# Kernel tuning notes

Measured on AMD Instinct MI355X. Metric: run time of the kernel, lower is better.

The kernel has to match this reference:

```python
import jax, jax.numpy as jnp
import numpy as np

T, B, I, H = 512, 32, 512, 512

def setup_inputs() -> dict:
    key = jax.random.key(0)
    k1, k2, k3 = jax.random.split(key, 3)
    x = jax.random.normal(k1, (T, B, I), dtype=jnp.float32)
    h0 = jnp.zeros((B, H), dtype=jnp.float32)
    W_ih = jax.random.normal(k2, (3 * H, I), dtype=jnp.float32) * (1.0 / np.sqrt(H))
    # diagonal recurrent weights, one vector per gate (r, z, n), uniform(-1, 1)
    w_hh = jax.random.uniform(k3, (3, H), dtype=jnp.float32, minval=-1.0, maxval=1.0)
    return {"x": x, "h0": h0, "W_ih": W_ih, "w_hh": w_hh}

def reference(x, h0, W_ih, w_hh):
    # Precompute input-side gate pre-activations for all timesteps: (T, B, 3H)
    gx = jnp.einsum('tbi,gi->tbg', x, W_ih)
    xr, xz, xn = jnp.split(gx, 3, axis=-1)  # each (T, B, H)
    w_r, w_z, w_n = w_hh[0], w_hh[1], w_hh[2]  # each (H,)

    def step(h, g):
        gr, gz, gn = g
        r = jax.nn.sigmoid(gr + w_r * h)
        z = jax.nn.sigmoid(gz + w_z * h)
        n = jnp.tanh(gn + r * (w_n * h))
        h_new = (1.0 - z) * n + z * h
        return h_new, h_new

    h_last, out = jax.lax.scan(step, h0, (xr, xz, xn))
    # out: (T, B, H) all hidden states; h_last: (1, B, H) final state (GRU convention)
    return out, h_last[None, :, :]
```

## Files before the change

### kernel.cpp

```cpp
#include <hip/hip_runtime.h>
#include <hip/hip_bf16.h>
#include <stdint.h>

#define T_DIM 512
#define B_DIM 32
#define K_DIM 512
#define H_DIM 512
#define N_DIM 1536
#define M_DIM 16384

typedef __bf16 bf16_t;
typedef bf16_t bf16x8 __attribute__((ext_vector_type(8)));
typedef float floatx4 __attribute__((ext_vector_type(4)));

#define LOG2E 1.442695041f
#define TWO_LOG2E 2.885390082f

__device__ __forceinline__ unsigned int f2bf_bits(float f) {
  uint32_t u = __builtin_bit_cast(uint32_t, f);
  u += 0x7FFFu + ((u >> 16) & 1u);
  return u >> 16;
}

__global__ void convert_both_kernel(const float* __restrict__ x,
                                    unsigned short* __restrict__ xb,
                                    const float* __restrict__ W,
                                    unsigned short* __restrict__ Wb) {
  int bid = blockIdx.x;
  const float* src;
  unsigned short* dst;
  int i;
  if (bid < 4096) {
    i = (bid * 256 + threadIdx.x) * 8;
    src = x + i;
    dst = xb + i;
  } else {
    i = ((bid - 4096) * 256 + threadIdx.x) * 8;
    int n = i >> 9;
    int k = i & 511;
    int p6 = n / 6;
    int sub = n - p6 * 6;
    int hodd = (sub >= 3) ? 1 : 0;
    int g = sub - hodd * 3;
    int h = p6 * 2 + hodd;
    src = W + ((g << 9) + h) * 512 + k;
    dst = Wb + i;
  }
  const float4* p = (const float4*)src;
  float4 f0 = p[0];
  float4 f1 = p[1];
  uint4 v;
  v.x = f2bf_bits(f0.x) | (f2bf_bits(f0.y) << 16);
  v.y = f2bf_bits(f0.z) | (f2bf_bits(f0.w) << 16);
  v.z = f2bf_bits(f1.x) | (f2bf_bits(f1.y) << 16);
  v.w = f2bf_bits(f1.z) | (f2bf_bits(f1.w) << 16);
  *(uint4*)dst = v;
}

__global__ __launch_bounds__(512, 4) void gemm_bf16_kernel(
    const unsigned short* __restrict__ A, const unsigned short* __restrict__ Bm,
    _Float16* __restrict__ C) {
  __shared__ bf16_t smem[24576];
  const int tid = threadIdx.x;
  const int lane = tid & 63;
  const int w = tid >> 6;
  const int id = blockIdx.x;
  const int swz = (id & 7) * 96 + (id >> 3);
  const int mIdx = swz / 12;
  const int nIdx = swz - mIdx * 12;
  const int tileM = mIdx * 256;
  const int tileN = nIdx * 128;
  const int waveM = w & 3;
  const int waveN = w >> 2;
  const int lm = lane & 15;
  const int lg = lane >> 4;

  floatx4 acc[4][4] = {};

  for (int k0 = 0; k0 < K_DIM; k0 += 64) {
#pragma unroll
    for (int g = 0; g < 4; ++g) {
      int s = g * 512 + tid;
      int row = s >> 3;
      int kc = (s & 7) ^ (row & 7);
      bf16_t* la = smem + (g * 512 + w * 64) * 8;
      const unsigned short* ga = A + (size_t)(tileM + row) * K_DIM + k0 + kc * 8;
      __builtin_amdgcn_global_load_lds(
          (const __attribute__((address_space(1))) unsigned int*)ga,
          (__attribute__((address_space(3))) unsigned int*)la, 16, 0, 0);
    }
#pragma unroll
    for (int g = 0; g < 2; ++g) {
      int s = g * 512 + tid;
      int row = s >> 3;
      int kc = (s & 7) ^ (row & 7);
      bf16_t* lb = smem + 16384 + (g * 512 + w * 64) * 8;
      const unsigned short* gb = Bm + (size_t)(tileN + row) * K_DIM + k0 + kc * 8;
      __builtin_amdgcn_global_load_lds(
          (const __attribute__((address_space(1))) unsigned int*)gb,
          (__attribute__((address_space(3))) unsigned int*)lb, 16, 0, 0);
    }
    __syncthreads();

#pragma unroll
    for (int ks = 0; ks < 2; ++ks) {
      bf16x8 af[4], bfg[4];
#pragma unroll
      for (int i = 0; i < 4; ++i) {
        int row = waveM * 64 + i * 16 + lm;
        int c = ks * 4 + lg;
        af[i] = *(const bf16x8*)(smem + row * 64 + (c ^ (row & 7)) * 8);
      }
#pragma unroll
      for (int j = 0; j < 4; ++j) {
        int row = waveN * 64 + j * 16 + lm;
        int c = ks * 4 + lg;
        bfg[j] = *(const bf16x8*)(smem + 16384 + row * 64 + (c ^ (row & 7)) * 8);
      }
#pragma unroll
      for (int i = 0; i < 4; ++i)
#pragma unroll
        for (int j = 0; j < 4; ++j)
          acc[i][j] = __builtin_amdgcn_mfma_f32_16x16x32_bf16(af[i], bfg[j],
                                                              acc[i][j], 0, 0, 0);
    }
    __syncthreads();
  }

  _Float16* ep = (_Float16*)smem + w * 2048;
  const int q = lm;
  const int rgrp = lane >> 4;
  const size_t crow0 = (size_t)(tileM + waveM * 64);
  const int ccol = tileN + waveN * 64 + q * 4;
#pragma unroll
  for (int p = 0; p < 2; ++p) {
#pragma unroll
    for (int il = 0; il < 2; ++il) {
      const int i = 2 * p + il;
#pragma unroll
      for (int j = 0; j < 4; ++j) {
        const int cl = lm + j * 16;
        const int sub = (tileN + waveN * 64 + cl) % 6;
        const float scl = (sub == 2 || sub == 5) ? TWO_LOG2E : -LOG2E;
#pragma unroll
        for (int r = 0; r < 4; ++r) {
          int rl = (lane >> 4) * 4 + r + 16 * il;
          ep[rl * 64 + cl] = (_Float16)(scl * acc[i][j][r]);
        }
      }
    }
#pragma unroll
    for (int k = 0; k < 8; ++k) {
      int rl = rgrp + 4 * k;
      uint2 v = *(const uint2*)(ep + rl * 64 + q * 4);
      *(uint2*)(C + (crow0 + p * 32 + rl) * N_DIM + ccol) = v;
    }
  }
}

__global__ __launch_bounds__(64) void indgru_scan_kernel(
    const _Float16* __restrict__ gx, const float* __restrict__ h0,
    const float* __restrict__ w_hh, float* __restrict__ out,
    float* __restrict__ hlast) {
  const int idx = blockIdx.x * 64 + threadIdx.x;
  const int b = idx >> 9;
  const int h = idx & (H_DIM - 1);
  const float wr = -LOG2E * w_hh[h];
  const float wz = -LOG2E * w_hh[H_DIM + h];
  const float wn = TWO_LOG2E * w_hh[2 * H_DIM + h];
  const int sh = (h & 1) << 4;
  float hv = h0[idx];

  const char* base = (const char*)(gx + (size_t)b * N_DIM + (h >> 1) * 6) + ((h & 1) << 2);
  float* outp = out + (size_t)b * H_DIM + h;

  constexpr int D = 32;
  constexpr size_t TSTRIDE = (size_t)B_DIM * N_DIM * sizeof(_Float16);
  uint2 pq[D];
#pragma unroll
  for (int t = 0; t < D; ++t)
    pq[t] = *(const uint2*)(base + (size_t)t * TSTRIDE);

  auto cvt16 = [](uint32_t bits) {
    return (float)__builtin_bit_cast(_Float16, (unsigned short)bits);
  };

  for (int t0 = 0; t0 < T_DIM - D; t0 += D) {
#pragma unroll
    for (int s = 0; s < D; ++s) {
      const int t = t0 + s;
      uint2 qv = pq[s];
      pq[s] = *(const uint2*)(base + (size_t)(t + D) * TSTRIDE);
      asm volatile("" ::: "memory");
      uint64_t v = (((uint64_t)qv.y << 32) | qv.x) >> sh;
      float gr = cvt16((uint32_t)v);
      float gz = cvt16((uint32_t)(v >> 16));
      float gn = cvt16((uint32_t)(v >> 32));
      float ar = fmaf(wr, hv, gr);
      float az = fmaf(wz, hv, gz);
      float t1 = wn * hv;
      float er = __builtin_amdgcn_exp2f(ar);
      float ez = __builtin_amdgcn_exp2f(az);
      float r = __builtin_amdgcn_rcpf(1.0f + er);
      float z = __builtin_amdgcn_rcpf(1.0f + ez);
      float en = __builtin_amdgcn_exp2f(fmaf(r, t1, gn));
      float u = __builtin_amdgcn_rcpf(1.0f + en);
      float n = fmaf(-2.0f, u, 1.0f);
      float zh = z * hv;
      float omz = 1.0f - z;
      hv = fmaf(n, omz, zh);
      outp[(size_t)t * (B_DIM * H_DIM)] = hv;
    }
  }
#pragma unroll
  for (int s = 0; s < D; ++s) {
    const int t = T_DIM - D + s;
    uint2 qv = pq[s];
    uint64_t v = (((uint64_t)qv.y << 32) | qv.x) >> sh;
    float gr = cvt16((uint32_t)v);
    float gz = cvt16((uint32_t)(v >> 16));
    float gn = cvt16((uint32_t)(v >> 32));
    float ar = fmaf(wr, hv, gr);
    float az = fmaf(wz, hv, gz);
    float t1 = wn * hv;
    float er = __builtin_amdgcn_exp2f(ar);
    float ez = __builtin_amdgcn_exp2f(az);
    float r = __builtin_amdgcn_rcpf(1.0f + er);
    float z = __builtin_amdgcn_rcpf(1.0f + ez);
    float en = __builtin_amdgcn_exp2f(fmaf(r, t1, gn));
    float u = __builtin_amdgcn_rcpf(1.0f + en);
    float n = fmaf(-2.0f, u, 1.0f);
    float zh = z * hv;
    float omz = 1.0f - z;
    hv = fmaf(n, omz, zh);
    outp[(size_t)t * (B_DIM * H_DIM)] = hv;
  }
  hlast[idx] = hv;
}

extern "C" void kernel_launch(void* const* d_in, const int* in_sizes, int n_in,
                              void* d_out, int out_size, void* d_ws, size_t ws_size,
                              hipStream_t stream) {
  const float* x    = (const float*)d_in[0];
  const float* h0   = (const float*)d_in[1];
  const float* W_ih = (const float*)d_in[2];
  const float* w_hh = (const float*)d_in[3];

  float* out = (float*)d_out;
  float* hlast = out + (size_t)T_DIM * B_DIM * H_DIM;

  char* ws = (char*)d_ws;
  unsigned short* xb = (unsigned short*)ws;
  unsigned short* Wb = (unsigned short*)(ws + 16777216);
  _Float16* gx = (_Float16*)(ws + 16777216 + 1572864);

  convert_both_kernel<<<4480, 256, 0, stream>>>(x, xb, W_ih, Wb);

  gemm_bf16_kernel<<<768, 512, 0, stream>>>(xb, Wb, gx);

  indgru_scan_kernel<<<256, 64, 0, stream>>>(gx, h0, w_hh, out, hlast);
}
```

Before: 149.9 us.

## Enlarge GEMM tile to 256x384 with 2x4 wave layout and 256 blocks

The GEMM block tile grows from 256x128 to 256x384. Each wave now computes a 128x96 sub-tile, 8x6 MFMA accumulators, with the A fragment loaded inside the row loop. The grid shrinks to 256 blocks, about one per CU, so A is reloaded fewer times across N tiles and MFMA work per LDS load rises. In exchange, register pressure is much higher, LDS per block grows, occupancy drops to 2 blocks, and the epilogue is restructured with padded staging rows.

```diff
diff --git a/kernel.cpp b/kernel.cpp
--- a/kernel.cpp
+++ b/kernel.cpp
@@ -57,25 +57,25 @@
   *(uint4*)dst = v;
 }
 
-__global__ __launch_bounds__(512, 4) void gemm_bf16_kernel(
+__global__ __launch_bounds__(512, 2) void gemm_bf16_kernel(
     const unsigned short* __restrict__ A, const unsigned short* __restrict__ Bm,
     _Float16* __restrict__ C) {
-  __shared__ bf16_t smem[24576];
+  __shared__ bf16_t smem[40960];
   const int tid = threadIdx.x;
   const int lane = tid & 63;
   const int w = tid >> 6;
   const int id = blockIdx.x;
-  const int swz = (id & 7) * 96 + (id >> 3);
-  const int mIdx = swz / 12;
-  const int nIdx = swz - mIdx * 12;
+  const int swz = (id & 7) * 32 + (id >> 3);
+  const int mIdx = swz >> 2;
+  const int nIdx = swz & 3;
   const int tileM = mIdx * 256;
-  const int tileN = nIdx * 128;
-  const int waveM = w & 3;
-  const int waveN = w >> 2;
+  const int tileN = nIdx * 384;
+  const int waveM = w >> 2;
+  const int waveN = w & 3;
   const int lm = lane & 15;
   const int lg = lane >> 4;
 
-  floatx4 acc[4][4] = {};
+  floatx4 acc[8][6] = {};
 
   for (int k0 = 0; k0 < K_DIM; k0 += 64) {
 #pragma unroll
@@ -90,7 +90,7 @@
           (__attribute__((address_space(3))) unsigned int*)la, 16, 0, 0);
     }
 #pragma unroll
-    for (int g = 0; g < 2; ++g) {
+    for (int g = 0; g < 6; ++g) {
       int s = g * 512 + tid;
       int row = s >> 3;
       int kc = (s & 7) ^ (row & 7);
@@ -104,56 +104,53 @@
 
 #pragma unroll
     for (int ks = 0; ks < 2; ++ks) {
-      bf16x8 af[4], bfg[4];
-#pragma unroll
-      for (int i = 0; i < 4; ++i) {
-        int row = waveM * 64 + i * 16 + lm;
-        int c = ks * 4 + lg;
-        af[i] = *(const bf16x8*)(smem + row * 64 + (c ^ (row & 7)) * 8);
+      bf16x8 bfg[6];
+      const int c = ks * 4 + lg;
+#pragma unroll
+      for (int j = 0; j < 6; ++j) {
+        int row = waveN * 96 + j * 16 + lm;
+        bfg[j] = *(const bf16x8*)(smem + 16384 + row * 64 + ((c ^ (row & 7)) << 3));
       }
 #pragma unroll
-      for (int j = 0; j < 4; ++j) {
-        int row = waveN * 64 + j * 16 + lm;
-        int c = ks * 4 + lg;
-        bfg[j] = *(const bf16x8*)(smem + 16384 + row * 64 + (c ^ (row & 7)) * 8);
+      for (int i = 0; i < 8; ++i) {
+        int row = waveM * 128 + i * 16 + lm;
+        bf16x8 af = *(const bf16x8*)(smem + row * 64 + ((c ^ (row & 7)) << 3));
+#pragma unroll
+        for (int j = 0; j < 6; ++j)
+          acc[i][j] = __builtin_amdgcn_mfma_f32_16x16x32_bf16(af, bfg[j],
+                                                              acc[i][j], 0, 0, 0);
       }
-#pragma unroll
-      for (int i = 0; i < 4; ++i)
-#pragma unroll
-        for (int j = 0; j < 4; ++j)
-          acc[i][j] = __builtin_amdgcn_mfma_f32_16x16x32_bf16(af[i], bfg[j],
-                                                              acc[i][j], 0, 0, 0);
     }
     __syncthreads();
   }
 
-  _Float16* ep = (_Float16*)smem + w * 2048;
-  const int q = lm;
-  const int rgrp = lane >> 4;
-  const size_t crow0 = (size_t)(tileM + waveM * 64);
-  const int ccol = tileN + waveN * 64 + q * 4;
-#pragma unroll
-  for (int p = 0; p < 2; ++p) {
-#pragma unroll
-    for (int il = 0; il < 2; ++il) {
-      const int i = 2 * p + il;
-#pragma unroll
-      for (int j = 0; j < 4; ++j) {
+  _Float16* ep = (_Float16*)smem + w * 3200;
+  const size_t crow0 = (size_t)(tileM + waveM * 128);
+  const int ccol0 = tileN + waveN * 96;
+#pragma unroll
+  for (int p = 0; p < 4; ++p) {
+#pragma unroll
+    for (int ih = 0; ih < 2; ++ih) {
+      const int i = 2 * p + ih;
+#pragma unroll
+      for (int j = 0; j < 6; ++j) {
         const int cl = lm + j * 16;
-        const int sub = (tileN + waveN * 64 + cl) % 6;
+        const int sub = (ccol0 + cl) % 6;
         const float scl = (sub == 2 || sub == 5) ? TWO_LOG2E : -LOG2E;
 #pragma unroll
         for (int r = 0; r < 4; ++r) {
-          int rl = (lane >> 4) * 4 + r + 16 * il;
-          ep[rl * 64 + cl] = (_Float16)(scl * acc[i][j][r]);
+          int rl = (lane >> 4) * 4 + r + 16 * ih;
+          ep[rl * 100 + cl] = (_Float16)(scl * acc[i][j][r]);
         }
       }
     }
 #pragma unroll
-    for (int k = 0; k < 8; ++k) {
-      int rl = rgrp + 4 * k;
-      uint2 v = *(const uint2*)(ep + rl * 64 + q * 4);
-      *(uint2*)(C + (crow0 + p * 32 + rl) * N_DIM + ccol) = v;
+    for (int rnd = 0; rnd < 12; ++rnd) {
+      int idx = rnd * 64 + lane;
+      int row = idx / 24;
+      int cu = idx - row * 24;
+      uint2 v = *(const uint2*)(ep + row * 100 + cu * 4);
+      *(uint2*)(C + (crow0 + p * 32 + row) * N_DIM + ccol0 + cu * 4) = v;
     }
   }
 }
@@ -256,7 +253,7 @@
 
   convert_both_kernel<<<4480, 256, 0, stream>>>(x, xb, W_ih, Wb);
 
-  gemm_bf16_kernel<<<768, 512, 0, stream>>>(xb, Wb, gx);
+  gemm_bf16_kernel<<<256, 512, 0, stream>>>(xb, Wb, gx);
 
   indgru_scan_kernel<<<256, 64, 0, stream>>>(gx, h0, w_hh, out, hlast);
 }
```

After: 151.7 us. No clear change (+1.2%).

## Fuse GEMM and scan into one kernel with per-band flag synchronization

Applied to the files above, without the earlier changes.

Merges the input-projection GEMM and the recurrent scan into a single launch. 32 scan blocks of 512 threads spin on per-band completion counters that GEMM blocks increment with release atomics, so the scan can start on early timesteps while later GEMM tiles are still being computed. GEMM tiles are remapped so each 256-row time band is covered by one XCD group, and the epilogue LDS stride is padded to 68 to reduce bank conflicts. The costs are that scan blocks occupy CUs while they spin, there is a deadlock risk if scan blocks get scheduled but GEMM blocks cannot run, and the scan prefetch depth drops from 32 timesteps to 8.

```diff
diff --git a/kernel.cpp b/kernel.cpp
--- a/kernel.cpp
+++ b/kernel.cpp
@@ -15,6 +15,7 @@
 
 #define LOG2E 1.442695041f
 #define TWO_LOG2E 2.885390082f
+#define SCAN_BLOCKS 32
 
 __device__ __forceinline__ unsigned int f2bf_bits(float f) {
   uint32_t u = __builtin_bit_cast(uint32_t, f);
@@ -25,8 +26,10 @@
 __global__ void convert_both_kernel(const float* __restrict__ x,
                                     unsigned short* __restrict__ xb,
                                     const float* __restrict__ W,
-                                    unsigned short* __restrict__ Wb) {
+                                    unsigned short* __restrict__ Wb,
+                                    uint32_t* __restrict__ flags) {
   int bid = blockIdx.x;
+  if (bid == 0 && threadIdx.x < 64) flags[threadIdx.x] = 0u;
   const float* src;
   unsigned short* dst;
   int i;
@@ -57,185 +60,193 @@
   *(uint4*)dst = v;
 }
 
-__global__ __launch_bounds__(512, 4) void gemm_bf16_kernel(
+__global__ __launch_bounds__(512, 4) void fused_gemm_scan(
     const unsigned short* __restrict__ A, const unsigned short* __restrict__ Bm,
-    _Float16* __restrict__ C) {
+    _Float16* __restrict__ C, uint32_t* __restrict__ flags,
+    const float* __restrict__ h0, const float* __restrict__ w_hh,
+    float* __restrict__ out, float* __restrict__ hlast) {
   __shared__ bf16_t smem[24576];
   const int tid = threadIdx.x;
-  const int lane = tid & 63;
-  const int w = tid >> 6;
-  const int id = blockIdx.x;
-  const int swz = (id & 7) * 96 + (id >> 3);
-  const int mIdx = swz / 12;
-  const int nIdx = swz - mIdx * 12;
-  const int tileM = mIdx * 256;
-  const int tileN = nIdx * 128;
-  const int waveM = w & 3;
-  const int waveN = w >> 2;
-  const int lm = lane & 15;
-  const int lg = lane >> 4;
-
-  floatx4 acc[4][4] = {};
-
-  for (int k0 = 0; k0 < K_DIM; k0 += 64) {
-#pragma unroll
-    for (int g = 0; g < 4; ++g) {
-      int s = g * 512 + tid;
-      int row = s >> 3;
-      int kc = (s & 7) ^ (row & 7);
-      bf16_t* la = smem + (g * 512 + w * 64) * 8;
-      const unsigned short* ga = A + (size_t)(tileM + row) * K_DIM + k0 + kc * 8;
-      __builtin_amdgcn_global_load_lds(
-          (const __attribute__((address_space(1))) unsigned int*)ga,
-          (__attribute__((address_space(3))) unsigned int*)la, 16, 0, 0);
+
+  if (blockIdx.x >= SCAN_BLOCKS) {
+    const int lane = tid & 63;
+    const int w = tid >> 6;
+    const int id = blockIdx.x - SCAN_BLOCKS;
+    const int xcd = id & 7;
+    const int q = id >> 3;
+    const int bq = q / 12;
+    const int nIdx = q - bq * 12;
+    const int band = bq * 8 + xcd;
+    const int tileM = band * 256;
+    const int tileN = nIdx * 128;
+    const int waveM = w & 3;
+    const int waveN = w >> 2;
+    const int lm = lane & 15;
+    const int lg = lane >> 4;
+
+    floatx4 acc[4][4] = {};
+
+    for (int k0 = 0; k0 < K_DIM; k0 += 64) {
+#pragma unroll
+      for (int g = 0; g < 4; ++g) {
+        int s = g * 512 + tid;
+        int row = s >> 3;
+        int kc = (s & 7) ^ (row & 7);
+        bf16_t* la = smem + (g * 512 + w * 64) * 8;
+        const unsigned short* ga = A + (size_t)(tileM + row) * K_DIM + k0 + kc * 8;
+        __builtin_amdgcn_global_load_lds(
+            (const __attribute__((address_space(1))) unsigned int*)ga,
+            (__attribute__((address_space(3))) unsigned int*)la, 16, 0, 0);
+      }
+#pragma unroll
+      for (int g = 0; g < 2; ++g) {
+        int s = g * 512 + tid;
+        int row = s >> 3;
+        int kc = (s & 7) ^ (row & 7);
+        bf16_t* lb = smem + 16384 + (g * 512 + w * 64) * 8;
+        const unsigned short* gb = Bm + (size_t)(tileN + row) * K_DIM + k0 + kc * 8;
+        __builtin_amdgcn_global_load_lds(
+            (const __attribute__((address_space(1))) unsigned int*)gb,
+            (__attribute__((address_space(3))) unsigned int*)lb, 16, 0, 0);
+      }
+      __syncthreads();
+
+#pragma unroll
+      for (int ks = 0; ks < 2; ++ks) {
+        bf16x8 af[4], bfg[4];
+#pragma unroll
+        for (int i = 0; i < 4; ++i) {
+          int row = waveM * 64 + i * 16 + lm;
+          int c = ks * 4 + lg;
+          af[i] = *(const bf16x8*)(smem + row * 64 + ((c ^ (row & 7)) << 3));
+        }
+#pragma unroll
+        for (int j = 0; j < 4; ++j) {
+          int row = waveN * 64 + j * 16 + lm;
+          int c = ks * 4 + lg;
+          bfg[j] = *(const bf16x8*)(smem + 16384 + row * 64 + ((c ^ (row & 7)) << 3));
+        }
+#pragma unroll
+        for (int i = 0; i < 4; ++i)
+#pragma unroll
+          for (int j = 0; j < 4; ++j)
+            acc[i][j] = __builtin_amdgcn_mfma_f32_16x16x32_bf16(af[i], bfg[j],
+                                                                acc[i][j], 0, 0, 0);
+      }
+      __syncthreads();
     }
-#pragma unroll
-    for (int g = 0; g < 2; ++g) {
-      int s = g * 512 + tid;
-      int row = s >> 3;
-      int kc = (s & 7) ^ (row & 7);
-      bf16_t* lb = smem + 16384 + (g * 512 + w * 64) * 8;
-      const unsigned short* gb = Bm + (size_t)(tileN + row) * K_DIM + k0 + kc * 8;
-      __builtin_amdgcn_global_load_lds(
-          (const __attribute__((address_space(1))) unsigned int*)gb,
-          (__attribute__((address_space(3))) unsigned int*)lb, 16, 0, 0);
+
+    _Float16* ep = (_Float16*)smem + w * 2176;
+    const int qq = lm;
+    const int rgrp = lane >> 4;
+    const size_t crow0 = (size_t)(tileM + waveM * 64);
+    const int ccol = tileN + waveN * 64 + qq * 4;
+#pragma unroll
+    for (int p = 0; p < 2; ++p) {
+#pragma unroll
+      for (int il = 0; il < 2; ++il) {
+        const int i = 2 * p + il;
+#pragma unroll
+        for (int j = 0; j < 4; ++j) {
+          const int cl = lm + j * 16;
+          const int sub = (tileN + waveN * 64 + cl) % 6;
+          const float scl = (sub == 2 || sub == 5) ? TWO_LOG2E : -LOG2E;
+#pragma unroll
+          for (int r = 0; r < 4; ++r) {
+            int rl = (lane >> 4) * 4 + r + 16 * il;
+            ep[rl * 68 + cl] = (_Float16)(scl * acc[i][j][r]);
+          }
+        }
+      }
+#pragma unroll
+      for (int k = 0; k < 8; ++k) {
+        int rl = rgrp + 4 * k;
+        uint2 v = *(const uint2*)(ep + rl * 68 + qq * 4);
+        *(uint2*)(C + (crow0 + p * 32 + rl) * N_DIM + ccol) = v;
+      }
     }
+
+    __threadfence();
     __syncthreads();
-
-#pragma unroll
-    for (int ks = 0; ks < 2; ++ks) {
-      bf16x8 af[4], bfg[4];
-#pragma unroll
-      for (int i = 0; i < 4; ++i) {
-        int row = waveM * 64 + i * 16 + lm;
-        int c = ks * 4 + lg;
-        af[i] = *(const bf16x8*)(smem + row * 64 + (c ^ (row & 7)) * 8);
-      }
-#pragma unroll
-      for (int j = 0; j < 4; ++j) {
-        int row = waveN * 64 + j * 16 + lm;
-        int c = ks * 4 + lg;
-        bfg[j] = *(const bf16x8*)(smem + 16384 + row * 64 + (c ^ (row & 7)) * 8);
-      }
-#pragma unroll
-      for (int i = 0; i < 4; ++i)
-#pragma unroll
-        for (int j = 0; j < 4; ++j)
-          acc[i][j] = __builtin_amdgcn_mfma_f32_16x16x32_bf16(af[i], bfg[j],
-                                                              acc[i][j], 0, 0, 0);
+    if (tid == 0)
+      __hip_atomic_fetch_add(&flags[band], 1u, __ATOMIC_RELEASE,
+                             __HIP_MEMORY_SCOPE_AGENT);
+  } else {
+    const int idx = blockIdx.x * 512 + tid;
+    const int b = idx >> 9;
+    const int h = idx & (H_DIM - 1);
+    const float wr = -LOG2E * w_hh[h];
+    const float wz = -LOG2E * w_hh[H_DIM + h];
+    const float wn = TWO_LOG2E * w_hh[2 * H_DIM + h];
+    const int sh = (h & 1) << 4;
+    float hv = h0[idx];
+    const char* base =
+        (const char*)(C + (size_t)b * N_DIM + (h >> 1) * 6) + ((h & 1) << 2);
+    float* outp = out + (size_t)b * H_DIM + h;
+    constexpr size_t TSTRIDE = (size_t)B_DIM * N_DIM * sizeof(_Float16);
+
+    auto wait_band = [&](int bd) {
+      const uint32_t* f = flags + bd;
+      if ((tid & 63) == 0) {
+        while (__hip_atomic_load(f, __ATOMIC_RELAXED,
+                                 __HIP_MEMORY_SCOPE_AGENT) < 12u)
+          __builtin_amdgcn_s_sleep(2);
+      }
+      __builtin_amdgcn_wave_barrier();
+      uint32_t v =
+          __hip_atomic_load(f, __ATOMIC_ACQUIRE, __HIP_MEMORY_SCOPE_AGENT);
+      asm volatile("" ::"v"(v) : "memory");
+    };
+    auto cvt16 = [](uint32_t bits) {
+      return (float)__builtin_bit_cast(_Float16, (unsigned short)bits);
+    };
+    uint2 pqA[8], pqB[8];
+    auto load8 = [&](uint2* dst, int bd) {
+#pragma unroll
+      for (int s = 0; s < 8; ++s)
+        dst[s] = *(const uint2*)(base + (size_t)(bd * 8 + s) * TSTRIDE);
+      asm volatile("" ::: "memory");
+    };
+    auto compute8 = [&](const uint2* pq, int bd) {
+#pragma unroll
+      for (int s = 0; s < 8; ++s) {
+        const int t = bd * 8 + s;
+        uint2 qv = pq[s];
+        uint64_t v = (((uint64_t)qv.y << 32) | qv.x) >> sh;
+        float gr = cvt16((uint32_t)v);
+        float gz = cvt16((uint32_t)(v >> 16));
+        float gn = cvt16((uint32_t)(v >> 32));
+        float ar = fmaf(wr, hv, gr);
+        float az = fmaf(wz, hv, gz);
+        float t1 = wn * hv;
+        float er = __builtin_amdgcn_exp2f(ar);
+        float ez = __builtin_amdgcn_exp2f(az);
+        float r = __builtin_amdgcn_rcpf(1.0f + er);
+        float z = __builtin_amdgcn_rcpf(1.0f + ez);
+        float en = __builtin_amdgcn_exp2f(fmaf(r, t1, gn));
+        float u = __builtin_amdgcn_rcpf(1.0f + en);
+        float n = fmaf(-2.0f, u, 1.0f);
+        float zh = z * hv;
+        float omz = 1.0f - z;
+        hv = fmaf(n, omz, zh);
+        outp[(size_t)t * (B_DIM * H_DIM)] = hv;
+      }
+    };
+
+    wait_band(0);
+    load8(pqA, 0);
+    for (int bb = 0; bb < 64; bb += 2) {
+      wait_band(bb + 1);
+      load8(pqB, bb + 1);
+      compute8(pqA, bb);
+      if (bb + 2 < 64) {
+        wait_band(bb + 2);
+        load8(pqA, bb + 2);
+      }
+      compute8(pqB, bb + 1);
     }
-    __syncthreads();
+    hlast[idx] = hv;
   }
-
-  _Float16* ep = (_Float16*)smem + w * 2048;
-  const int q = lm;
-  const int rgrp = lane >> 4;
-  const size_t crow0 = (size_t)(tileM + waveM * 64);
-  const int ccol = tileN + waveN * 64 + q * 4;
-#pragma unroll
-  for (int p = 0; p < 2; ++p) {
-#pragma unroll
-    for (int il = 0; il < 2; ++il) {
-      const int i = 2 * p + il;
-#pragma unroll
-      for (int j = 0; j < 4; ++j) {
-        const int cl = lm + j * 16;
-        const int sub = (tileN + waveN * 64 + cl) % 6;
-        const float scl = (sub == 2 || sub == 5) ? TWO_LOG2E : -LOG2E;
-#pragma unroll
-        for (int r = 0; r < 4; ++r) {
-          int rl = (lane >> 4) * 4 + r + 16 * il;
-          ep[rl * 64 + cl] = (_Float16)(scl * acc[i][j][r]);
-        }
-      }
-    }
-#pragma unroll
-    for (int k = 0; k < 8; ++k) {
-      int rl = rgrp + 4 * k;
-      uint2 v = *(const uint2*)(ep + rl * 64 + q * 4);
-      *(uint2*)(C + (crow0 + p * 32 + rl) * N_DIM + ccol) = v;
-    }
-  }
-}
-
-__global__ __launch_bounds__(64) void indgru_scan_kernel(
-    const _Float16* __restrict__ gx, const float* __restrict__ h0,
-    const float* __restrict__ w_hh, float* __restrict__ out,
-    float* __restrict__ hlast) {
-  const int idx = blockIdx.x * 64 + threadIdx.x;
-  const int b = idx >> 9;
-  const int h = idx & (H_DIM - 1);
-  const float wr = -LOG2E * w_hh[h];
-  const float wz = -LOG2E * w_hh[H_DIM + h];
-  const float wn = TWO_LOG2E * w_hh[2 * H_DIM + h];
-  const int sh = (h & 1) << 4;
-  float hv = h0[idx];
-
-  const char* base = (const char*)(gx + (size_t)b * N_DIM + (h >> 1) * 6) + ((h & 1) << 2);
-  float* outp = out + (size_t)b * H_DIM + h;
-
-  constexpr int D = 32;
-  constexpr size_t TSTRIDE = (size_t)B_DIM * N_DIM * sizeof(_Float16);
-  uint2 pq[D];
-#pragma unroll
-  for (int t = 0; t < D; ++t)
-    pq[t] = *(const uint2*)(base + (size_t)t * TSTRIDE);
-
-  auto cvt16 = [](uint32_t bits) {
-    return (float)__builtin_bit_cast(_Float16, (unsigned short)bits);
-  };
-
-  for (int t0 = 0; t0 < T_DIM - D; t0 += D) {
-#pragma unroll
-    for (int s = 0; s < D; ++s) {
-      const int t = t0 + s;
-      uint2 qv = pq[s];
-      pq[s] = *(const uint2*)(base + (size_t)(t + D) * TSTRIDE);
-      asm volatile("" ::: "memory");
-      uint64_t v = (((uint64_t)qv.y << 32) | qv.x) >> sh;
-      float gr = cvt16((uint32_t)v);
-      float gz = cvt16((uint32_t)(v >> 16));
-      float gn = cvt16((uint32_t)(v >> 32));
-      float ar = fmaf(wr, hv, gr);
-      float az = fmaf(wz, hv, gz);
-      float t1 = wn * hv;
-      float er = __builtin_amdgcn_exp2f(ar);
-      float ez = __builtin_amdgcn_exp2f(az);
-      float r = __builtin_amdgcn_rcpf(1.0f + er);
-      float z = __builtin_amdgcn_rcpf(1.0f + ez);
-      float en = __builtin_amdgcn_exp2f(fmaf(r, t1, gn));
-      float u = __builtin_amdgcn_rcpf(1.0f + en);
-      float n = fmaf(-2.0f, u, 1.0f);
-      float zh = z * hv;
-      float omz = 1.0f - z;
-      hv = fmaf(n, omz, zh);
-      outp[(size_t)t * (B_DIM * H_DIM)] = hv;
-    }
-  }
-#pragma unroll
-  for (int s = 0; s < D; ++s) {
-    const int t = T_DIM - D + s;
-    uint2 qv = pq[s];
-    uint64_t v = (((uint64_t)qv.y << 32) | qv.x) >> sh;
-    float gr = cvt16((uint32_t)v);
-    float gz = cvt16((uint32_t)(v >> 16));
-    float gn = cvt16((uint32_t)(v >> 32));
-    float ar = fmaf(wr, hv, gr);
-    float az = fmaf(wz, hv, gz);
-    float t1 = wn * hv;
-    float er = __builtin_amdgcn_exp2f(ar);
-    float ez = __builtin_amdgcn_exp2f(az);
-    float r = __builtin_amdgcn_rcpf(1.0f + er);
-    float z = __builtin_amdgcn_rcpf(1.0f + ez);
-    float en = __builtin_amdgcn_exp2f(fmaf(r, t1, gn));
-    float u = __builtin_amdgcn_rcpf(1.0f + en);
-    float n = fmaf(-2.0f, u, 1.0f);
-    float zh = z * hv;
-    float omz = 1.0f - z;
-    hv = fmaf(n, omz, zh);
-    outp[(size_t)t * (B_DIM * H_DIM)] = hv;
-  }
-  hlast[idx] = hv;
 }
 
 extern "C" void kernel_launch(void* const* d_in, const int* in_sizes, int n_in,
@@ -253,10 +264,10 @@
   unsigned short* xb = (unsigned short*)ws;
   unsigned short* Wb = (unsigned short*)(ws + 16777216);
   _Float16* gx = (_Float16*)(ws + 16777216 + 1572864);
-
-  convert_both_kernel<<<4480, 256, 0, stream>>>(x, xb, W_ih, Wb);
-
-  gemm_bf16_kernel<<<768, 512, 0, stream>>>(xb, Wb, gx);
-
-  indgru_scan_kernel<<<256, 64, 0, stream>>>(gx, h0, w_hh, out, hlast);
-}
+  uint32_t* flags = (uint32_t*)(ws + 16777216 + 1572864 + 50331648);
+
+  convert_both_kernel<<<4480, 256, 0, stream>>>(x, xb, W_ih, Wb, flags);
+
+  fused_gemm_scan<<<SCAN_BLOCKS + 768, 512, 0, stream>>>(
+      xb, Wb, gx, flags, h0, w_hh, out, hlast);
+}
```

New measurement: 447.8 us. 2.99x slower.
